# Optimization experiments

Measured on AMD Instinct MI355X. Metric: run time of the kernel, lower is better.

## Reference

```python
import jax, jax.numpy as jnp
import numpy as np

E, D_IN, D_OUT = 8, 1024, 1024
B, S = 4, 2048

def setup_inputs() -> dict:
    key = jax.random.key(0)
    k_x, k_g, k_gb, k_w = jax.random.split(key, 4)
    x = jax.random.normal(k_x, (B, S, D_IN), dtype=jnp.float32)
    gate_w = jax.random.normal(k_g, (D_IN, E), dtype=jnp.float32) * 0.02
    gate_b = jax.random.normal(k_gb, (E,), dtype=jnp.float32) * 0.02
    expert_w = jax.random.normal(k_w, (E, D_IN, D_OUT), dtype=jnp.float32) * 0.02
    return {"x": x, "gate_w": gate_w, "gate_b": gate_b, "expert_w": expert_w}

def reference(x, gate_w, gate_b, expert_w):
    # gate: softmax over experts
    gate_score = jax.nn.softmax(x @ gate_w + gate_b, axis=-1)        # [B,S,E]
    # all-expert dense GEMM: [B,S,E,out]
    expert_out = jnp.einsum('bsi,eio->bseo', x, expert_w)
    # gate-weighted combine: [B,S,out]
    out = jnp.einsum('bse,bseo->bso', gate_score, expert_out)
    return out
```

## Files before the change

kernel.cpp:

```cpp
#include <hip/hip_runtime.h>
#include <hip/hip_bf16.h>
#include <cstdint>

#define TOKENS 8192
#define DIN 1024
#define DOUT 1024
#define NE 8

typedef __bf16 bf16;
typedef __attribute__((ext_vector_type(8))) __bf16 bf16x8;
typedef __attribute__((ext_vector_type(4))) float floatx4;

__device__ __forceinline__ void async16(const void* gptr, void* lptr) {
  __builtin_amdgcn_global_load_lds(
      (const __attribute__((address_space(1))) void*)gptr,
      (__attribute__((address_space(3))) void*)lptr,
      16, 0, 0);
}

__global__ __launch_bounds__(256) void prep_kernel(
    const float* __restrict__ x, const float* __restrict__ gw,
    const float* __restrict__ gb, float* __restrict__ g,
    bf16* __restrict__ xb, const float* __restrict__ w,
    bf16* __restrict__ wt) {
  __shared__ __align__(16) float smem[NE * DIN];

  const int tid = threadIdx.x;
  if (blockIdx.x < 512) {
#pragma unroll
    for (int k = 0; k < 8; ++k) {
      const int base = (k * 256 + tid) * 4;
      const floatx4 v = *(const floatx4*)(gw + base);
#pragma unroll
      for (int m = 0; m < 4; ++m) {
        const int j = base + m;
        smem[(j & 7) * DIN + (j >> 3)] = v[m];
      }
    }
    __syncthreads();

    const int lane = tid & 63;
    const int wave = tid >> 6;
#pragma unroll
    for (int tt = 0; tt < 4; ++tt) {
      const int t = blockIdx.x * 16 + wave * 4 + tt;
      const float* xr = x + (size_t)t * DIN;
      bf16* xbr = xb + (size_t)t * DIN;

      float acc[NE];
#pragma unroll
      for (int e = 0; e < NE; ++e) acc[e] = 0.f;

#pragma unroll
      for (int it = 0; it < 4; ++it) {
        const int i = it * 256 + lane * 4;
        const floatx4 xv = *(const floatx4*)(xr + i);
        union { bf16 b[4]; uint64_t u; } cv;
#pragma unroll
        for (int m = 0; m < 4; ++m) cv.b[m] = (bf16)xv[m];
        *(uint64_t*)(xbr + i) = cv.u;
#pragma unroll
        for (int e = 0; e < NE; ++e) {
          const floatx4 wv = *(const floatx4*)(smem + e * DIN + i);
          acc[e] += xv[0] * wv[0] + xv[1] * wv[1] + xv[2] * wv[2] + xv[3] * wv[3];
        }
      }
#pragma unroll
      for (int e = 0; e < NE; ++e)
#pragma unroll
        for (int off = 32; off > 0; off >>= 1)
          acc[e] += __shfl_xor(acc[e], off, 64);

      float lg[NE];
      float mx = -3.0e38f;
#pragma unroll
      for (int e = 0; e < NE; ++e) { lg[e] = acc[e] + gb[e]; mx = fmaxf(mx, lg[e]); }
      float s = 0.f;
#pragma unroll
      for (int e = 0; e < NE; ++e) { lg[e] = __expf(lg[e] - mx); s += lg[e]; }
      const float inv = 1.f / s;
      if (lane == 0) {
        floatx4 o0, o1;
#pragma unroll
        for (int e = 0; e < 4; ++e) { o0[e] = lg[e] * inv; o1[e] = lg[e + 4] * inv; }
        *(floatx4*)(g + (size_t)t * NE) = o0;
        *(floatx4*)(g + (size_t)t * NE + 4) = o1;
      }
    }
  } else {
    float (*tile)[65] = (float(*)[65])smem;
    const int bt = blockIdx.x - 512;
    const int e = bt & 7;
    const int j = bt >> 3;
    const int i0 = (j >> 4) * 64;
    const int o0 = (j & 15) * 64;
    const int c4 = (tid & 15) * 4;
    const int r = tid >> 4;

    const float* src = w + ((size_t)e * DIN + i0) * DOUT + o0;
#pragma unroll
    for (int rr = r; rr < 64; rr += 16) {
      const floatx4 v = *(const floatx4*)(src + (size_t)rr * DOUT + c4);
      tile[rr][c4] = v[0]; tile[rr][c4 + 1] = v[1];
      tile[rr][c4 + 2] = v[2]; tile[rr][c4 + 3] = v[3];
    }
    __syncthreads();
    bf16* dst = wt + ((size_t)e * DOUT + o0) * DIN + i0;
#pragma unroll
    for (int rr = r; rr < 64; rr += 16) {
      union { bf16 b[4]; uint64_t u; } cv;
#pragma unroll
      for (int jj = 0; jj < 4; ++jj) cv.b[jj] = (bf16)tile[c4 + jj][rr];
      *(uint64_t*)(dst + (size_t)rr * DIN + c4) = cv.u;
    }
  }
}

__global__ __launch_bounds__(256, 2) void moe_gemm(
    const bf16* __restrict__ xb, const bf16* __restrict__ wt,
    const float* __restrict__ g, float* __restrict__ out) {
  __shared__ __align__(16) bf16 As[2][128 * 64];
  __shared__ __align__(16) bf16 Bs[2][128 * 64];

  const int tid = threadIdx.x;
  const int c = blockIdx.x & 7;
  const int jj = blockIdx.x >> 3;
  const int bm = (c >> 1) * 16 + (jj & 15);
  const int bn = (c & 1) * 4 + (jj >> 4);
  const int lane = tid & 63;
  const int wave = tid >> 6;
  const int wm = wave >> 1, wn = wave & 1;
  const int lr = lane & 15, lq = lane >> 4;

  const int srow = tid >> 3;
  const int scol = (((tid & 7) ^ (srow & 7)) << 3);
  const int kx = lr & 7;

  const bf16* const agp = xb + (size_t)(bm * 128 + srow) * DIN + scol;
  const bf16* const bgp = wt + (size_t)(bn * 128 + srow) * DIN + scol;

  const floatx4 fzero = {0.f, 0.f, 0.f, 0.f};
  floatx4 accF[4][4], accE[4][4];
#pragma unroll
  for (int im = 0; im < 4; ++im)
#pragma unroll
    for (int in = 0; in < 4; ++in) { accF[im][in] = fzero; accE[im][in] = fzero; }

  const int tok0 = bm * 128 + wm * 64;

  {
    bf16* const alp = &As[0][tid * 8];
    bf16* const blp = &Bs[0][tid * 8];
#pragma unroll
    for (int j = 0; j < 4; ++j)
      async16(agp + (size_t)(32 * j) * DIN, alp + j * 2048);
#pragma unroll
    for (int j = 0; j < 4; ++j)
      async16(bgp + (size_t)(32 * j) * DIN, blp + j * 2048);
  }
  __syncthreads();

  for (int t = 0; t < 128; ++t) {
    const int cur = t & 1;
    const bf16* const Ab = &As[cur][0];
    const bf16* const Bb = &Bs[cur][0];

    bf16x8 av[2][4], bv[2][4];
#pragma unroll
    for (int kk = 0; kk < 2; ++kk) {
      const int kg = ((kk * 4 + lq) ^ kx) << 3;
#pragma unroll
      for (int im = 0; im < 4; ++im)
        av[kk][im] = *(const bf16x8*)(Ab + (wm * 64 + im * 16 + lr) * 64 + kg);
#pragma unroll
      for (int in = 0; in < 4; ++in)
        bv[kk][in] = *(const bf16x8*)(Bb + (wn * 64 + in * 16 + lr) * 64 + kg);
    }

    const int t1 = t + 1;
    bf16* const alp = &As[cur ^ 1][tid * 8];
    bf16* const blp = &Bs[cur ^ 1][tid * 8];
    const size_t koff = (size_t)((t1 & 15) << 6);
    if (t1 < 128) {
#pragma unroll
      for (int j = 0; j < 4; ++j)
        async16(agp + koff + (size_t)(32 * j) * DIN, alp + j * 2048);
    }

    __builtin_amdgcn_s_setprio(1);
#pragma unroll
    for (int im = 0; im < 4; ++im)
#pragma unroll
      for (int in = 0; in < 4; ++in)
        accE[im][in] = __builtin_amdgcn_mfma_f32_16x16x32_bf16(
            av[0][im], bv[0][in], accE[im][in], 0, 0, 0);
    __builtin_amdgcn_s_setprio(0);

    if (t1 < 128) {
      const bf16* const bsrc = bgp + ((size_t)(t1 >> 4) << 20) + koff;
#pragma unroll
      for (int j = 0; j < 4; ++j)
        async16(bsrc + (size_t)(32 * j) * DIN, blp + j * 2048);
    }

    __builtin_amdgcn_s_setprio(1);
#pragma unroll
    for (int im = 0; im < 4; ++im)
#pragma unroll
      for (int in = 0; in < 4; ++in)
        accE[im][in] = __builtin_amdgcn_mfma_f32_16x16x32_bf16(
            av[1][im], bv[1][in], accE[im][in], 0, 0, 0);
    __builtin_amdgcn_s_setprio(0);

    if ((t & 15) == 15) {
      const int e = t >> 4;
#pragma unroll
      for (int im = 0; im < 4; ++im) {
        float gv[4];
#pragma unroll
        for (int r = 0; r < 4; ++r)
          gv[r] = g[(size_t)(tok0 + im * 16 + lq * 4 + r) * NE + e];
#pragma unroll
        for (int in = 0; in < 4; ++in)
#pragma unroll
          for (int r = 0; r < 4; ++r) {
            accF[im][in][r] += gv[r] * accE[im][in][r];
            accE[im][in][r] = 0.f;
          }
      }
    }

    __syncthreads();
  }

#pragma unroll
  for (int im = 0; im < 4; ++im)
#pragma unroll
    for (int in = 0; in < 4; ++in) {
      const int col = bn * 128 + wn * 64 + in * 16 + lr;
#pragma unroll
      for (int r = 0; r < 4; ++r)
        out[(size_t)(tok0 + im * 16 + lq * 4 + r) * DOUT + col] =
            accF[im][in][r];
    }
}

extern "C" void kernel_launch(void* const* d_in, const int* in_sizes, int n_in,
                              void* d_out, int out_size, void* d_ws,
                              size_t ws_size, hipStream_t stream) {
  const float* x  = (const float*)d_in[0];
  const float* gw = (const float*)d_in[1];
  const float* gb = (const float*)d_in[2];
  const float* w  = (const float*)d_in[3];
  float* out = (float*)d_out;

  char* ws = (char*)d_ws;
  float* g  = (float*)ws;
  bf16* xb  = (bf16*)(ws + 262144);
  bf16* wt  = (bf16*)(ws + 262144 + (size_t)TOKENS * DIN * 2);

  prep_kernel<<<2560, 256, 0, stream>>>(x, gw, gb, g, xb, w, wt);
  moe_gemm<<<512, 256, 0, stream>>>(xb, wt, g, out);
}
```

Measured before the change: 233.0 us.

## Reorder GEMM loop to iterate experts inside K tiles, reusing A fragments

The main loop now runs experts inside each K tile. The A tile is loaded into registers once per K step and reused across all 8 experts, instead of being reloaded for every expert. Gate weights are staged in shared memory up front, and the per-step expert partial is combined with the gate after every step, replacing a combine once per expert. The trade is 64 extra FMAs per step per thread and a gate LDS read each step, but the accE accumulators no longer live across steps.

```diff
diff --git a/kernel.cpp b/kernel.cpp
--- a/kernel.cpp
+++ b/kernel.cpp
@@ -121,6 +121,7 @@
     const float* __restrict__ g, float* __restrict__ out) {
   __shared__ __align__(16) bf16 As[2][128 * 64];
   __shared__ __align__(16) bf16 Bs[2][128 * 64];
+  __shared__ __align__(16) float gT[NE * 128];
 
   const int tid = threadIdx.x;
   const int c = blockIdx.x & 7;
@@ -140,14 +141,20 @@
   const bf16* const bgp = wt + (size_t)(bn * 128 + srow) * DIN + scol;
 
   const floatx4 fzero = {0.f, 0.f, 0.f, 0.f};
-  floatx4 accF[4][4], accE[4][4];
+  floatx4 accF[4][4];
 #pragma unroll
   for (int im = 0; im < 4; ++im)
 #pragma unroll
-    for (int in = 0; in < 4; ++in) { accF[im][in] = fzero; accE[im][in] = fzero; }
+    for (int in = 0; in < 4; ++in) accF[im][in] = fzero;
 
   const int tok0 = bm * 128 + wm * 64;
 
+  {
+    const int tok = tid >> 1, eh = (tid & 1) * 4;
+    const floatx4 gv4 = *(const floatx4*)(g + (size_t)(bm * 128 + tok) * NE + eh);
+#pragma unroll
+    for (int m = 0; m < 4; ++m) gT[(eh + m) * 128 + tok] = gv4[m];
+  }
   {
     bf16* const alp = &As[0][tid * 8];
     bf16* const blp = &Bs[0][tid * 8];
@@ -160,49 +167,64 @@
   }
   __syncthreads();
 
-  for (int t = 0; t < 128; ++t) {
-    const int cur = t & 1;
-    const bf16* const Ab = &As[cur][0];
+  bf16x8 av[2][4];
+
+  for (int s = 0; s < 128; ++s) {
+    const int kt = s >> 3;
+    const int e = s & 7;
+    const int cur = s & 1;
+
+    if (e == 0) {
+      const bf16* const Ab = &As[kt & 1][0];
+#pragma unroll
+      for (int kk = 0; kk < 2; ++kk) {
+        const int kg = ((kk * 4 + lq) ^ kx) << 3;
+#pragma unroll
+        for (int im = 0; im < 4; ++im)
+          av[kk][im] = *(const bf16x8*)(Ab + (wm * 64 + im * 16 + lr) * 64 + kg);
+      }
+    }
     const bf16* const Bb = &Bs[cur][0];
-
-    bf16x8 av[2][4], bv[2][4];
+    bf16x8 bv[2][4];
 #pragma unroll
     for (int kk = 0; kk < 2; ++kk) {
       const int kg = ((kk * 4 + lq) ^ kx) << 3;
 #pragma unroll
-      for (int im = 0; im < 4; ++im)
-        av[kk][im] = *(const bf16x8*)(Ab + (wm * 64 + im * 16 + lr) * 64 + kg);
-#pragma unroll
       for (int in = 0; in < 4; ++in)
         bv[kk][in] = *(const bf16x8*)(Bb + (wn * 64 + in * 16 + lr) * 64 + kg);
     }
-
-    const int t1 = t + 1;
-    bf16* const alp = &As[cur ^ 1][tid * 8];
-    bf16* const blp = &Bs[cur ^ 1][tid * 8];
-    const size_t koff = (size_t)((t1 & 15) << 6);
-    if (t1 < 128) {
-#pragma unroll
-      for (int j = 0; j < 4; ++j)
-        async16(agp + koff + (size_t)(32 * j) * DIN, alp + j * 2048);
-    }
-
-    __builtin_amdgcn_s_setprio(1);
-#pragma unroll
-    for (int im = 0; im < 4; ++im)
-#pragma unroll
-      for (int in = 0; in < 4; ++in)
-        accE[im][in] = __builtin_amdgcn_mfma_f32_16x16x32_bf16(
-            av[0][im], bv[0][in], accE[im][in], 0, 0, 0);
-    __builtin_amdgcn_s_setprio(0);
-
-    if (t1 < 128) {
-      const bf16* const bsrc = bgp + ((size_t)(t1 >> 4) << 20) + koff;
+    floatx4 gvi[4];
+#pragma unroll
+    for (int im = 0; im < 4; ++im)
+      gvi[im] = *(const floatx4*)(gT + e * 128 + wm * 64 + im * 16 + lq * 4);
+
+    const int s1 = s + 1;
+    if (s1 < 128) {
+      const int e1 = s1 & 7, kt1 = s1 >> 3;
+      const bf16* const bsrc =
+          bgp + ((size_t)e1 << 20) + (size_t)kt1 * 64;
+      bf16* const blp = &Bs[cur ^ 1][tid * 8];
 #pragma unroll
       for (int j = 0; j < 4; ++j)
         async16(bsrc + (size_t)(32 * j) * DIN, blp + j * 2048);
     }
-
+    if (e == 0 && kt + 1 < 16) {
+      bf16* const alp = &As[(kt + 1) & 1][tid * 8];
+#pragma unroll
+      for (int j = 0; j < 4; ++j)
+        async16(agp + (size_t)(kt + 1) * 64 + (size_t)(32 * j) * DIN,
+                alp + j * 2048);
+    }
+
+    floatx4 accE[4][4];
+    __builtin_amdgcn_s_setprio(1);
+#pragma unroll
+    for (int im = 0; im < 4; ++im)
+#pragma unroll
+      for (int in = 0; in < 4; ++in)
+        accE[im][in] = __builtin_amdgcn_mfma_f32_16x16x32_bf16(
+            av[0][im], bv[0][in], fzero, 0, 0, 0);
+    __builtin_amdgcn_s_setprio(0);
     __builtin_amdgcn_s_setprio(1);
 #pragma unroll
     for (int im = 0; im < 4; ++im)
@@ -212,23 +234,13 @@
             av[1][im], bv[1][in], accE[im][in], 0, 0, 0);
     __builtin_amdgcn_s_setprio(0);
 
-    if ((t & 15) == 15) {
-      const int e = t >> 4;
-#pragma unroll
-      for (int im = 0; im < 4; ++im) {
-        float gv[4];
+#pragma unroll
+    for (int im = 0; im < 4; ++im)
+#pragma unroll
+      for (int in = 0; in < 4; ++in)
 #pragma unroll
         for (int r = 0; r < 4; ++r)
-          gv[r] = g[(size_t)(tok0 + im * 16 + lq * 4 + r) * NE + e];
-#pragma unroll
-        for (int in = 0; in < 4; ++in)
-#pragma unroll
-          for (int r = 0; r < 4; ++r) {
-            accF[im][in][r] += gv[r] * accE[im][in][r];
-            accE[im][in][r] = 0.f;
-          }
-      }
-    }
+          accF[im][in][r] += gvi[im][r] * accE[im][in][r];
 
     __syncthreads();
   }
```

After: 230.7 us. About the same (-1.0%).
